# Performance work log

Measured on AMD Instinct MI355X. Metric: run time of the kernel, lower is better.

## Reference

```python
import jax, jax.numpy as jnp
import numpy as np

D_MODEL = 1024
N_HEADS = 16
D_FF = 4096
EPS = 1e-5


def setup_inputs() -> dict:
    key = jax.random.key(0)
    ks = jax.random.split(key, 10)
    B, S, D, F = 4, 2048, D_MODEL, D_FF
    s = 0.02
    return {
        "x": jax.random.normal(ks[0], (B, S, D), jnp.float32),
        "Wq": jax.random.normal(ks[1], (D, D), jnp.float32) * s,
        "bq": jnp.zeros((D,), jnp.float32),
        "Wk": jax.random.normal(ks[2], (D, D), jnp.float32) * s,
        "bk": jnp.zeros((D,), jnp.float32),
        "Wv": jax.random.normal(ks[3], (D, D), jnp.float32) * s,
        "bv": jnp.zeros((D,), jnp.float32),
        "Wo": jax.random.normal(ks[4], (D, D), jnp.float32) * s,
        "bo": jnp.zeros((D,), jnp.float32),
        "ln1_g": jnp.ones((D,), jnp.float32),
        "ln1_b": jnp.zeros((D,), jnp.float32),
        "ln2_g": jnp.ones((D,), jnp.float32),
        "ln2_b": jnp.zeros((D,), jnp.float32),
        "W1": jax.random.normal(ks[5], (D, F), jnp.float32) * s,
        "b1": jnp.zeros((F,), jnp.float32),
        "W2": jax.random.normal(ks[6], (F, D), jnp.float32) * s,
        "b2": jnp.zeros((D,), jnp.float32),
    }


def _layernorm(x, g, b):
    mu = jnp.mean(x, axis=-1, keepdims=True)
    var = jnp.mean(jnp.square(x - mu), axis=-1, keepdims=True)
    return (x - mu) * jax.lax.rsqrt(var + EPS) * g + b


def _attention(x, Wq, bq, Wk, bk, Wv, bv, Wo, bo):
    B, S, D = x.shape
    H, dk = N_HEADS, D // N_HEADS
    q = (x @ Wq + bq).reshape(B, S, H, dk).transpose(0, 2, 1, 3)  # bhsd
    k = (x @ Wk + bk).reshape(B, S, H, dk).transpose(0, 2, 1, 3)
    v = (x @ Wv + bv).reshape(B, S, H, dk).transpose(0, 2, 1, 3)
    scale = 1.0 / np.sqrt(dk)
    scores = jnp.einsum("bhqd,bhkd->bhqk", q, k) * scale
    causal = jnp.tril(jnp.ones((S, S), bool))
    scores = jnp.where(causal, scores, -jnp.inf)
    attn = jax.nn.softmax(scores, axis=-1)
    out = jnp.einsum("bhqk,bhkd->bhqd", attn, v)
    out = out.transpose(0, 2, 1, 3).reshape(B, S, D)
    return out @ Wo + bo


def reference(x, Wq, bq, Wk, bk, Wv, bv, Wo, bo, ln1_g, ln1_b, ln2_g, ln2_b, W1, b1, W2, b2):
    # Pre-LN: x -> LN -> attn -> +x -> LN -> FFN -> +x  (dropout = eval/identity)
    attn_out = _attention(_layernorm(x, ln1_g, ln1_b), Wq, bq, Wk, bk, Wv, bv, Wo, bo)
    x = x + attn_out
    h = _layernorm(x, ln2_g, ln2_b)
    ffn = jax.nn.gelu(h @ W1 + b1, approximate=False) @ W2 + b2
    return x + ffn
```

## Files before the change

kernel.cpp:

```cpp
#include <hip/hip_runtime.h>
#include <hip/hip_bf16.h>
#include <math.h>

typedef __attribute__((ext_vector_type(8))) short short8;
typedef __attribute__((ext_vector_type(4))) float floatx4;
typedef __attribute__((ext_vector_type(4))) short short4v;
typedef __attribute__((ext_vector_type(2))) unsigned int uint2v;

#define D_MODEL 1024
#define N_HEADS 16
#define DK 64
#define D_FF 4096
#define BB 4
#define SS 2048
#define NTOK (BB * SS)
#define LN_EPS 1e-5f
#define SCL 0.18033688011112042f

static __device__ __forceinline__ short f2bf(float f) {
  union { float f; unsigned int u; } v;
  v.f = f;
  unsigned int u = v.u;
  unsigned int r = u + 0x7fffu + ((u >> 16) & 1u);
  return (short)(r >> 16);
}

#define GLL16(g, l)                                                            \
  __builtin_amdgcn_global_load_lds(                                            \
      (const __attribute__((address_space(1))) void*)(g),                      \
      (__attribute__((address_space(3))) void*)(l), 16, 0, 0)

__global__ __launch_bounds__(256) void ln_kernel(const float* __restrict__ x,
                                                 const float* __restrict__ g,
                                                 const float* __restrict__ b,
                                                 short* __restrict__ out) {
  int row = blockIdx.x;
  int t = threadIdx.x;
  const float4* rp = (const float4*)(x + (size_t)row * D_MODEL);
  float4 v = rp[t];
  float s = v.x + v.y + v.z + v.w;
  float ss = v.x * v.x + v.y * v.y + v.z * v.z + v.w * v.w;
#pragma unroll
  for (int off = 32; off >= 1; off >>= 1) {
    s += __shfl_xor(s, off, 64);
    ss += __shfl_xor(ss, off, 64);
  }
  __shared__ float red[8];
  int wv = t >> 6;
  if ((t & 63) == 0) { red[wv] = s; red[wv + 4] = ss; }
  __syncthreads();
  s = red[0] + red[1] + red[2] + red[3];
  ss = red[4] + red[5] + red[6] + red[7];
  float mu = s * (1.0f / D_MODEL);
  float var = ss * (1.0f / D_MODEL) - mu * mu;
  float rstd = rsqrtf(var + LN_EPS);
  float4 gv = ((const float4*)g)[t];
  float4 bv = ((const float4*)b)[t];
  short4v o;
  o.x = f2bf((v.x - mu) * rstd * gv.x + bv.x);
  o.y = f2bf((v.y - mu) * rstd * gv.y + bv.y);
  o.z = f2bf((v.z - mu) * rstd * gv.z + bv.z);
  o.w = f2bf((v.w - mu) * rstd * gv.w + bv.w);
  *(short4v*)(out + (size_t)row * D_MODEL + t * 4) = o;
}

__global__ __launch_bounds__(256) void wconvert_all(
    const float* __restrict__ Wq, const float* __restrict__ Wk,
    const float* __restrict__ Wv, const float* __restrict__ Wo,
    const float* __restrict__ W1, const float* __restrict__ W2,
    const float* __restrict__ bq, const float* __restrict__ bk,
    const float* __restrict__ bv,
    short* __restrict__ wqkv_t, short* __restrict__ wo_t,
    short* __restrict__ w1_t, short* __restrict__ w2_t,
    float* __restrict__ bqkv) {
  __shared__ float tile[64][65];
  int id = blockIdx.x;
  int t = threadIdx.x;
  if (id == 3072) {
    for (int i = t; i < 1024; i += 256) {
      bqkv[i] = bq[i];
      bqkv[1024 + i] = bk[i];
      bqkv[2048 + i] = bv[i];
    }
    return;
  }
  const float* W;
  short* Wt;
  int K, N, tid;
  if (id < 1024) {
    int wsel = id >> 8;
    tid = id & 255;
    K = 1024; N = 1024;
    W = wsel == 0 ? Wq : wsel == 1 ? Wk : wsel == 2 ? Wv : Wo;
    Wt = wsel < 3 ? wqkv_t + (size_t)wsel * 1024 * 1024 : wo_t;
  } else if (id < 2048) {
    tid = id - 1024; K = 1024; N = 4096; W = W1; Wt = w1_t;
  } else {
    tid = id - 2048; K = 4096; N = 1024; W = W2; Wt = w2_t;
  }
  int ntn = N >> 6;
  int n0 = (tid % ntn) * 64, k0 = (tid / ntn) * 64;
  int c = t & 63, r0 = t >> 6;
#pragma unroll
  for (int i = 0; i < 16; i++) {
    int r = r0 + i * 4;
    tile[r][c] = W[(size_t)(k0 + r) * N + n0 + c];
  }
  __syncthreads();
#pragma unroll
  for (int i = 0; i < 16; i++) {
    int r = r0 + i * 4;
    Wt[(size_t)(n0 + r) * K + k0 + c] = f2bf(tile[c][r]);
  }
}

template <int MODE>
__global__ __launch_bounds__(256, 4) void gemm_bt(const short* __restrict__ A,
                                                  const short* __restrict__ Bt,
                                                  const float* __restrict__ bias,
                                                  const float* __restrict__ res,
                                                  float* __restrict__ outf,
                                                  short* __restrict__ outb,
                                                  int M, int N, int K) {
  __shared__ short As[128 * 64];
  __shared__ short Bs[128 * 64];
  int t = threadIdx.x;
  int w = t >> 6, l = t & 63;
  int lm = l & 15, lq = l >> 4;
  int nx = gridDim.x;
  int id = blockIdx.y * nx + blockIdx.x;
  int xcd = id & 7;
  int k = id >> 3;
  int rows_per = gridDim.y >> 3;
  int mt = xcd * rows_per + k / nx;
  int nt = k - (k / nx) * nx;
  int m0 = mt * 128, n0 = nt * 128;
  floatx4 acc[4][4] = {};
  int l3 = l >> 3;
  int c7 = ((l & 7) ^ l3) * 8;
  const short* aA = A + (size_t)(m0 + w * 8 + l3) * K + c7;
  const short* aB = Bt + (size_t)(n0 + w * 8 + l3) * K + c7;
  int wm = (w & 1) * 64, wn = (w >> 1) * 64;
  int sw = lm & 7;

  for (int kt = 0; kt < K; kt += 64) {
#pragma unroll
    for (int j = 0; j < 4; j++) {
      GLL16(aA + (size_t)(j * 32) * K, As + (j * 32 + w * 8) * 64);
      GLL16(aB + (size_t)(j * 32) * K, Bs + (j * 32 + w * 8) * 64);
    }
    aA += 64;
    aB += 64;
    __syncthreads();
#pragma unroll
    for (int kk = 0; kk < 2; kk++) {
      int rdoff = ((kk * 4 + lq) ^ sw) * 8;
      short8 af[4], bfr[4];
#pragma unroll
      for (int mi = 0; mi < 4; mi++)
        af[mi] = *(const short8*)&As[(wm + mi * 16 + lm) * 64 + rdoff];
#pragma unroll
      for (int ni = 0; ni < 4; ni++)
        bfr[ni] = *(const short8*)&Bs[(wn + ni * 16 + lm) * 64 + rdoff];
#pragma unroll
      for (int mi = 0; mi < 4; mi++)
#pragma unroll
        for (int ni = 0; ni < 4; ni++)
          acc[mi][ni] = __builtin_amdgcn_mfma_f32_16x16x32_bf16(af[mi], bfr[ni],
                                                                acc[mi][ni], 0, 0, 0);
    }
    __syncthreads();
  }

#pragma unroll
  for (int mi = 0; mi < 4; mi++) {
#pragma unroll
    for (int ni = 0; ni < 4; ni++) {
      int col = n0 + wn + ni * 16 + lm;
      float bcol = bias[col];
#pragma unroll
      for (int r = 0; r < 4; r++) {
        int row = m0 + wm + mi * 16 + lq * 4 + r;
        float v = acc[mi][ni][r] + bcol;
        size_t idx = (size_t)row * N + col;
        if (MODE == 0) {
          outb[idx] = f2bf(v);
        } else if (MODE == 1) {
          outf[idx] = v + res[idx];
        } else {
          float vc = v + 0.044715f * v * v * v;
          float e = __builtin_amdgcn_exp2f(2.302265246314f * vc);
          float ge = v * e * __builtin_amdgcn_rcpf(e + 1.0f);
          outb[idx] = f2bf(ge);
        }
      }
    }
  }
}

__global__ __launch_bounds__(256) void vtrans(const short* __restrict__ qkv,
                                              short* __restrict__ vt) {
  __shared__ short Ls[64][72];
  int t = threadIdx.x;
  int s0 = blockIdx.x * 64;
  int bh = blockIdx.y;
  int b = bh >> 4, h = bh & 15;
  const short* vsrc = qkv + (size_t)b * SS * 3072 + 2048 + h * 64;
#pragma unroll
  for (int it = 0; it < 2; it++) {
    int idx = it * 256 + t;
    int sr = idx >> 3, ch = idx & 7;
    *(short8*)&Ls[sr][ch * 8] =
        *(const short8*)&vsrc[(size_t)(s0 + sr) * 3072 + ch * 8];
  }
  __syncthreads();
  int d = t >> 2, sb = (t & 3) * 16;
  short tmp[16];
#pragma unroll
  for (int j = 0; j < 16; j++) tmp[j] = Ls[sb + j][d];
  short8* dst = (short8*)&vt[(size_t)bh * DK * SS + (size_t)d * SS + s0 + sb];
  dst[0] = *(short8*)&tmp[0];
  dst[1] = *(short8*)&tmp[8];
}

__global__ __launch_bounds__(256, 3) void attn_kernel(const short* __restrict__ qkv,
                                                      const short* __restrict__ vt,
                                                      short* __restrict__ o) {
  __shared__ short Qs[128 * 64];
  __shared__ short Ks[64 * 64];
  __shared__ short Vs[64 * 64];
  __shared__ short Ps[128 * 72];
  int t = threadIdx.x, w = t >> 6, l = t & 63;
  int bh = blockIdx.x;
  int qi = 15 - blockIdx.y;
  int b = bh >> 4, h = bh & 15;
  const short* qbase = qkv + (size_t)b * SS * 3072 + h * DK;
  const short* kbase = qbase + 1024;
  const short* vbase = vt + (size_t)bh * DK * SS;
  short* obase = o + (size_t)b * SS * D_MODEL + h * DK;
  int l7 = l & 7, l3 = l >> 3;
  int c7 = (l7 ^ l3) * 8;
  int lm = l & 15, lq = l >> 4;
  int swq = lm & 7;
  int q0 = qi * 128;

#pragma unroll
  for (int j = 0; j < 4; j++) {
    int r8 = w * 32 + j * 8;
    GLL16(qbase + (size_t)(q0 + r8 + l3) * 3072 + c7, Qs + r8 * 64);
  }
  __syncthreads();
  short8 aq[2][2];
#pragma unroll
  for (int m = 0; m < 2; m++)
#pragma unroll
    for (int hf = 0; hf < 2; hf++)
      aq[m][hf] = *(const short8*)&Qs[(w * 32 + m * 16 + lm) * 64 +
                                      ((hf * 4 + lq) ^ swq) * 8];

  floatx4 accO[2][4] = {};
  float lst[2] = {0.f, 0.f};
  int qrow[2] = {q0 + w * 32 + lm, q0 + w * 32 + 16 + lm};
  int wrow_min = q0 + w * 32;
  int wrow_max = wrow_min + 31;
  int ntile = 2 * qi + 2;
  for (int kt = 0; kt < ntile; kt++) {
    int k0 = kt * 64;
    __syncthreads();
#pragma unroll
    for (int j = 0; j < 2; j++) {
      int r8 = (w * 2 + j) * 8;
      GLL16(kbase + (size_t)(k0 + r8 + l3) * 3072 + c7, Ks + r8 * 64);
      GLL16(vbase + (size_t)(r8 + l3) * SS + k0 + c7, Vs + r8 * 64);
    }
    __syncthreads();

    if (k0 <= wrow_max) {
      floatx4 sc[4][2];
#pragma unroll
      for (int sb = 0; sb < 4; sb++) {
        short8 k0f = *(const short8*)&Ks[(sb * 16 + lm) * 64 + (lq ^ swq) * 8];
        short8 k1f =
            *(const short8*)&Ks[(sb * 16 + lm) * 64 + ((4 + lq) ^ swq) * 8];
#pragma unroll
        for (int m = 0; m < 2; m++) {
          floatx4 z = {};
          z = __builtin_amdgcn_mfma_f32_16x16x32_bf16(k0f, aq[m][0], z, 0, 0, 0);
          z = __builtin_amdgcn_mfma_f32_16x16x32_bf16(k1f, aq[m][1], z, 0, 0, 0);
          sc[sb][m] = z;
        }
      }
      if (k0 + 63 <= wrow_min) {
#pragma unroll
        for (int sb = 0; sb < 4; sb++)
#pragma unroll
          for (int m = 0; m < 2; m++)
#pragma unroll
            for (int r = 0; r < 4; r++) {
              float pv = exp2f(sc[sb][m][r] * SCL);
              sc[sb][m][r] = pv;
              lst[m] += pv;
            }
      } else {
#pragma unroll
        for (int sb = 0; sb < 4; sb++) {
          int sbase = k0 + sb * 16 + lq * 4;
#pragma unroll
          for (int m = 0; m < 2; m++)
#pragma unroll
            for (int r = 0; r < 4; r++) {
              float pv = (sbase + r > qrow[m]) ? 0.f : exp2f(sc[sb][m][r] * SCL);
              sc[sb][m][r] = pv;
              lst[m] += pv;
            }
        }
      }
#pragma unroll
      for (int m = 0; m < 2; m++)
#pragma unroll
        for (int sb = 0; sb < 4; sb++) {
          union { float f; unsigned int u; } c0, c1, c2, c3;
          c0.f = sc[sb][m][0]; c1.f = sc[sb][m][1];
          c2.f = sc[sb][m][2]; c3.f = sc[sb][m][3];
          uint2v pk;
          pk.x = (c0.u >> 16) | (c1.u & 0xFFFF0000u);
          pk.y = (c2.u >> 16) | (c3.u & 0xFFFF0000u);
          *(uint2v*)&Ps[(w * 32 + m * 16 + lm) * 72 + sb * 16 + lq * 4] = pk;
        }
      short8 pa[2][2];
#pragma unroll
      for (int m = 0; m < 2; m++)
#pragma unroll
        for (int hf = 0; hf < 2; hf++)
          pa[m][hf] =
              *(const short8*)&Ps[(w * 32 + m * 16 + lm) * 72 + hf * 32 + lq * 8];
#pragma unroll
      for (int nb = 0; nb < 4; nb++) {
        short8 v0f = *(const short8*)&Vs[(nb * 16 + lm) * 64 + (lq ^ swq) * 8];
        short8 v1f =
            *(const short8*)&Vs[(nb * 16 + lm) * 64 + ((4 + lq) ^ swq) * 8];
#pragma unroll
        for (int m = 0; m < 2; m++) {
          accO[m][nb] = __builtin_amdgcn_mfma_f32_16x16x32_bf16(pa[m][0], v0f,
                                                                accO[m][nb], 0, 0, 0);
          accO[m][nb] = __builtin_amdgcn_mfma_f32_16x16x32_bf16(pa[m][1], v1f,
                                                                accO[m][nb], 0, 0, 0);
        }
      }
    }
  }
#pragma unroll
  for (int m = 0; m < 2; m++) {
    float s = lst[m];
    s += __shfl_xor(s, 16, 64);
    s += __shfl_xor(s, 32, 64);
    float inv = 1.0f / s;
#pragma unroll
    for (int r = 0; r < 4; r++) {
      float invr = __shfl(inv, (l & 48) | (lq * 4 + r), 64);
      int rowg = q0 + w * 32 + m * 16 + lq * 4 + r;
#pragma unroll
      for (int nb = 0; nb < 4; nb++)
        obase[(size_t)rowg * D_MODEL + nb * 16 + lm] = f2bf(accO[m][nb][r] * invr);
    }
  }
}

extern "C" void kernel_launch(void* const* d_in, const int* in_sizes, int n_in,
                              void* d_out, int out_size, void* d_ws, size_t ws_size,
                              hipStream_t stream) {
  const float* x = (const float*)d_in[0];
  const float* Wq = (const float*)d_in[1];
  const float* bq = (const float*)d_in[2];
  const float* Wk = (const float*)d_in[3];
  const float* bk = (const float*)d_in[4];
  const float* Wv = (const float*)d_in[5];
  const float* bv = (const float*)d_in[6];
  const float* Wo = (const float*)d_in[7];
  const float* bo = (const float*)d_in[8];
  const float* ln1g = (const float*)d_in[9];
  const float* ln1b = (const float*)d_in[10];
  const float* ln2g = (const float*)d_in[11];
  const float* ln2b = (const float*)d_in[12];
  const float* W1 = (const float*)d_in[13];
  const float* b1 = (const float*)d_in[14];
  const float* W2 = (const float*)d_in[15];
  const float* b2 = (const float*)d_in[16];
  float* out = (float*)d_out;

  short* wqkv_t = (short*)d_ws;
  short* wo_t = wqkv_t + 3072 * 1024;
  short* w1_t = wo_t + 1024 * 1024;
  short* w2_t = w1_t + 4096 * 1024;
  float* bqkv = (float*)(w2_t + 1024 * 4096);
  short* h_bf = (short*)(bqkv + 3072);
  short* qkvb = h_bf + (size_t)NTOK * D_MODEL;
  short* vtg = qkvb + (size_t)NTOK * 3072;
  short* ffn1 = qkvb;

  wconvert_all<<<3073, 256, 0, stream>>>(Wq, Wk, Wv, Wo, W1, W2, bq, bk, bv,
                                         wqkv_t, wo_t, w1_t, w2_t, bqkv);

  ln_kernel<<<NTOK, 256, 0, stream>>>(x, ln1g, ln1b, h_bf);

  gemm_bt<0><<<dim3(24, 64), 256, 0, stream>>>(h_bf, wqkv_t, bqkv, nullptr, nullptr,
                                               qkvb, NTOK, 3072, 1024);

  vtrans<<<dim3(SS / 64, 64), 256, 0, stream>>>(qkvb, vtg);

  attn_kernel<<<dim3(64, 16), 256, 0, stream>>>(qkvb, vtg, h_bf);

  gemm_bt<1><<<dim3(8, 64), 256, 0, stream>>>(h_bf, wo_t, bo, x, out, nullptr,
                                              NTOK, 1024, 1024);

  ln_kernel<<<NTOK, 256, 0, stream>>>(out, ln2g, ln2b, h_bf);

  gemm_bt<2><<<dim3(32, 64), 256, 0, stream>>>(h_bf, w1_t, b1, nullptr, nullptr,
                                               ffn1, NTOK, 4096, 1024);

  gemm_bt<1><<<dim3(8, 64), 256, 0, stream>>>(ffn1, w2_t, b2, out, out, nullptr,
                                              NTOK, 1024, 4096);
}
```

Baseline: 469.4 us.

## Fold softmax scale into Wq and compute row sums via MFMA ones-column

Pre-scales Wq and bq by the softmax log2 scale during weight conversion, which removes the per-score multiply in attention and lets it use the raw hardware exp2. The softmax denominator is now taken from an extra MFMA against a ones row stored in padded V shared memory, replacing the per-element scalar accumulation and cross-lane shuffles. Bf16 packing uses a byte-permute instruction, and the final normalisation uses a hardware reciprocal. The row sums are now accumulated from bf16-truncated probabilities, and the approximate exp2 and rcp trade a little accuracy for fewer instructions.

```diff
diff --git a/kernel.cpp b/kernel.cpp
--- a/kernel.cpp
+++ b/kernel.cpp
@@ -78,7 +78,7 @@
   int t = threadIdx.x;
   if (id == 3072) {
     for (int i = t; i < 1024; i += 256) {
-      bqkv[i] = bq[i];
+      bqkv[i] = bq[i] * SCL;
       bqkv[1024 + i] = bk[i];
       bqkv[2048 + i] = bv[i];
     }
@@ -87,12 +87,14 @@
   const float* W;
   short* Wt;
   int K, N, tid;
+  float scale = 1.0f;
   if (id < 1024) {
     int wsel = id >> 8;
     tid = id & 255;
     K = 1024; N = 1024;
     W = wsel == 0 ? Wq : wsel == 1 ? Wk : wsel == 2 ? Wv : Wo;
     Wt = wsel < 3 ? wqkv_t + (size_t)wsel * 1024 * 1024 : wo_t;
+    if (wsel == 0) scale = SCL;
   } else if (id < 2048) {
     tid = id - 1024; K = 1024; N = 4096; W = W1; Wt = w1_t;
   } else {
@@ -110,7 +112,7 @@
 #pragma unroll
   for (int i = 0; i < 16; i++) {
     int r = r0 + i * 4;
-    Wt[(size_t)(n0 + r) * K + k0 + c] = f2bf(tile[c][r]);
+    Wt[(size_t)(n0 + r) * K + k0 + c] = f2bf(tile[c][r] * scale);
   }
 }
 
@@ -228,7 +230,7 @@
                                                       short* __restrict__ o) {
   __shared__ short Qs[128 * 64];
   __shared__ short Ks[64 * 64];
-  __shared__ short Vs[64 * 64];
+  __shared__ short Vs[80 * 64];
   __shared__ short Ps[128 * 72];
   int t = threadIdx.x, w = t >> 6, l = t & 63;
   int bh = blockIdx.x;
@@ -244,6 +246,13 @@
   int swq = lm & 7;
   int q0 = qi * 128;
 
+  {
+    int r = 64 + (t >> 4);
+    int c = (t & 15) * 4;
+    short val = (r == 64) ? (short)0x3F80 : (short)0;
+    short4v vv = {val, val, val, val};
+    *(short4v*)&Vs[r * 64 + c] = vv;
+  }
 #pragma unroll
   for (int j = 0; j < 4; j++) {
     int r8 = w * 32 + j * 8;
@@ -259,7 +268,7 @@
                                       ((hf * 4 + lq) ^ swq) * 8];
 
   floatx4 accO[2][4] = {};
-  float lst[2] = {0.f, 0.f};
+  floatx4 accL[2] = {};
   int qrow[2] = {q0 + w * 32 + lm, q0 + w * 32 + 16 + lm};
   int wrow_min = q0 + w * 32;
   int wrow_max = wrow_min + 31;
@@ -296,11 +305,8 @@
 #pragma unroll
           for (int m = 0; m < 2; m++)
 #pragma unroll
-            for (int r = 0; r < 4; r++) {
-              float pv = exp2f(sc[sb][m][r] * SCL);
-              sc[sb][m][r] = pv;
-              lst[m] += pv;
-            }
+            for (int r = 0; r < 4; r++)
+              sc[sb][m][r] = __builtin_amdgcn_exp2f(sc[sb][m][r]);
       } else {
 #pragma unroll
         for (int sb = 0; sb < 4; sb++) {
@@ -308,11 +314,10 @@
 #pragma unroll
           for (int m = 0; m < 2; m++)
 #pragma unroll
-            for (int r = 0; r < 4; r++) {
-              float pv = (sbase + r > qrow[m]) ? 0.f : exp2f(sc[sb][m][r] * SCL);
-              sc[sb][m][r] = pv;
-              lst[m] += pv;
-            }
+            for (int r = 0; r < 4; r++)
+              sc[sb][m][r] = (sbase + r > qrow[m])
+                                 ? 0.f
+                                 : __builtin_amdgcn_exp2f(sc[sb][m][r]);
         }
       }
 #pragma unroll
@@ -323,8 +328,8 @@
           c0.f = sc[sb][m][0]; c1.f = sc[sb][m][1];
           c2.f = sc[sb][m][2]; c3.f = sc[sb][m][3];
           uint2v pk;
-          pk.x = (c0.u >> 16) | (c1.u & 0xFFFF0000u);
-          pk.y = (c2.u >> 16) | (c3.u & 0xFFFF0000u);
+          pk.x = __builtin_amdgcn_perm(c1.u, c0.u, 0x07060302u);
+          pk.y = __builtin_amdgcn_perm(c3.u, c2.u, 0x07060302u);
           *(uint2v*)&Ps[(w * 32 + m * 16 + lm) * 72 + sb * 16 + lq * 4] = pk;
         }
       short8 pa[2][2];
@@ -334,6 +339,13 @@
         for (int hf = 0; hf < 2; hf++)
           pa[m][hf] =
               *(const short8*)&Ps[(w * 32 + m * 16 + lm) * 72 + hf * 32 + lq * 8];
+      short8 o0 = *(const short8*)&Vs[(64 + lm) * 64 + (lq ^ swq) * 8];
+      short8 o1 = *(const short8*)&Vs[(64 + lm) * 64 + ((4 + lq) ^ swq) * 8];
+#pragma unroll
+      for (int m = 0; m < 2; m++) {
+        accL[m] = __builtin_amdgcn_mfma_f32_16x16x32_bf16(pa[m][0], o0, accL[m], 0, 0, 0);
+        accL[m] = __builtin_amdgcn_mfma_f32_16x16x32_bf16(pa[m][1], o1, accL[m], 0, 0, 0);
+      }
 #pragma unroll
       for (int nb = 0; nb < 4; nb++) {
         short8 v0f = *(const short8*)&Vs[(nb * 16 + lm) * 64 + (lq ^ swq) * 8];
@@ -351,13 +363,10 @@
   }
 #pragma unroll
   for (int m = 0; m < 2; m++) {
-    float s = lst[m];
-    s += __shfl_xor(s, 16, 64);
-    s += __shfl_xor(s, 32, 64);
-    float inv = 1.0f / s;
 #pragma unroll
     for (int r = 0; r < 4; r++) {
-      float invr = __shfl(inv, (l & 48) | (lq * 4 + r), 64);
+      float lv = __shfl(accL[m][r], l & 48, 64);
+      float invr = __builtin_amdgcn_rcpf(lv);
       int rowg = q0 + w * 32 + m * 16 + lq * 4 + r;
 #pragma unroll
       for (int nb = 0; nb < 4; nb++)
```

Result: no change. 465.8 us (-0.8%).
